# Kernel optimization log

Hardware: AMD Instinct MI355X
Metric: run time of the kernel (lower is better)

## Reference

```python
import jax, jax.numpy as jnp
import numpy as np

# dims: H heads, D=word_size (d_model), E=embed_dim per head, N=seq_len=n, K=linformer k
H, D, E, N, K = 16, 1024, 64, 4096, 256


def setup_inputs() -> dict:
    key = jax.random.key(0)
    ks = jax.random.split(key, 9)
    s = 0.02  # init scale for weights
    return {
        "x":  jax.random.normal(ks[0], (N, D), jnp.float32),
        # per-head QKV linears: torch Linear weight is (out=E, in=D), bias (E,)
        "Wq": jax.random.normal(ks[1], (H, E, D), jnp.float32) * s,
        "bq": jnp.zeros((H, E), jnp.float32),
        "Wk": jax.random.normal(ks[2], (H, E, D), jnp.float32) * s,
        "bk": jnp.zeros((H, E), jnp.float32),
        "Wv": jax.random.normal(ks[3], (H, E, D), jnp.float32) * s,
        "bv": jnp.zeros((H, E), jnp.float32),
        # per-head E/F sequence projections: Linear(n=N, k=K) -> weight (K, N), bias (K,)
        "Ew": jax.random.normal(ks[4], (H, K, N), jnp.float32) * s,
        "Eb": jnp.zeros((H, K), jnp.float32),
        "Fw": jax.random.normal(ks[5], (H, K, N), jnp.float32) * s,
        "Fb": jnp.zeros((H, K), jnp.float32),
        # output projection: Linear(H*E, E, bias=False) -> weight (E, H*E)
        "Wo": jax.random.normal(ks[6], (E, H * E), jnp.float32) * s,
    }


def reference(x, Wq, bq, Wk, bk, Wv, bv, Ew, Eb, Fw, Fb, Wo):
    # per-head Q/K/V projections, batched over heads: (H, N, E)
    q = jnp.einsum('nd,hed->hne', x, Wq) + bq[:, None, :]
    k = jnp.einsum('nd,hed->hne', x, Wk) + bk[:, None, :]
    v = jnp.einsum('nd,hed->hne', x, Wv) + bv[:, None, :]
    # low-rank sequence-length projection of K and V: (H, K, E)
    kp = jnp.einsum('hjn,hne->hje', Ew, k) + Eb[:, :, None]
    vp = jnp.einsum('hjn,hne->hje', Fw, v) + Fb[:, :, None]
    # scaled dot-product attention against projected keys: (H, N, K)
    score = jnp.einsum('hne,hje->hnj', q, kp) / jnp.sqrt(jnp.float32(E))
    attn = jax.nn.softmax(score, axis=-1)
    z = jnp.einsum('hnj,hje->hne', attn, vp)  # (H, N, E)
    # concat heads along feature dim (matches torch.cat(dim=1)): (N, H*E)
    zs = jnp.transpose(z, (1, 0, 2)).reshape(N, H * E)
    # final projection Linear(H*E, E, bias=False)
    return zs @ Wo.T  # (N, E)
```

## Files before the change

kernel.cpp:

```cpp
#include <hip/hip_runtime.h>
#include <hip/hip_bf16.h>

typedef __attribute__((ext_vector_type(4))) float f32x4;
typedef __attribute__((ext_vector_type(8))) short s16x8;
typedef __attribute__((ext_vector_type(4))) short s16x4;
typedef unsigned short u16;


__device__ __forceinline__ f32x4 mfma16(s16x8 a, s16x8 b, f32x4 c) {
    return __builtin_amdgcn_mfma_f32_16x16x32_bf16(a, b, c, 0, 0, 0);
}

__device__ __forceinline__ u16 bf(float f) {
    union { float f; unsigned u; } x; x.f = f;
    return (u16)((x.u + 0x7fffu + ((x.u >> 16) & 1u)) >> 16);
}
__device__ __forceinline__ unsigned pkbf(float a, float b) {
    union { float f; unsigned u; } x, y; x.f = a; y.f = b;
    unsigned ra = x.u + 0x7fffu + ((x.u >> 16) & 1u);
    unsigned rb = y.u + 0x7fffu + ((y.u >> 16) & 1u);
    return (ra >> 16) | (rb & 0xffff0000u);
}
__device__ __forceinline__ s16x8 cvt8(f32x4 lo, f32x4 hi) {
    union { s16x8 v; unsigned u[4]; } r;
    r.u[0] = pkbf(lo.x, lo.y);
    r.u[1] = pkbf(lo.z, lo.w);
    r.u[2] = pkbf(hi.x, hi.y);
    r.u[3] = pkbf(hi.z, hi.w);
    return r.v;
}

__device__ __forceinline__ void gl_lds16(const u16* g, u16* l) {
    __builtin_amdgcn_global_load_lds(
        (const __attribute__((address_space(1))) unsigned*)g,
        (__attribute__((address_space(3))) unsigned*)l, 16, 0, 0);
}


__global__ __launch_bounds__(256) void cvt_kernel(const float* __restrict__ src,
                                                  u16* __restrict__ dst, int n4) {
    int i = blockIdx.x * 256 + threadIdx.x;
    if (i < n4) {
        f32x4 v = ((const f32x4*)src)[i];
        union { s16x4 v; unsigned u[2]; } r;
        r.u[0] = pkbf(v.x, v.y);
        r.u[1] = pkbf(v.z, v.w);
        ((s16x4*)dst)[i] = r.v;
    }
}


__global__ __launch_bounds__(256, 2) void qkv_kernel(
        const u16* __restrict__ xb, const u16* __restrict__ wb,
        const float* __restrict__ bq, const float* __restrict__ bk,
        const float* __restrict__ bv,
        u16* __restrict__ qo, u16* __restrict__ kTo, u16* __restrict__ vTo) {
    __shared__ u16 As[128 * 32];
    __shared__ u16 Bs[128 * 32];
    int bx   = blockIdx.x % 24;
    int by   = blockIdx.x / 24;
    int tid  = threadIdx.x;
    int lane = tid & 63, w = tid >> 6;
    int l15  = lane & 15, quad = lane >> 4;
    int wr   = w >> 1, wc = w & 1;

    const u16* Ag = xb + (size_t)(by * 128 + (tid >> 2)) * 1024 + (tid & 3) * 8;
    const u16* Bg = wb + (size_t)(bx * 128 + (tid >> 2)) * 1024 + (tid & 3) * 8;
    u16* Al = As + tid * 8;
    u16* Bl = Bs + tid * 8;

    const u16* abase = As + (wr * 64 + l15) * 32 + quad * 8;
    const u16* bbase = Bs + (wc * 64 + l15) * 32 + quad * 8;

    f32x4 acc[4][4] = {};
    for (int k0 = 0; k0 < 1024; k0 += 32) {
        gl_lds16(Ag + k0, Al);
        gl_lds16(Ag + 64 * 1024 + k0, Al + 64 * 32);
        gl_lds16(Bg + k0, Bl);
        gl_lds16(Bg + 64 * 1024 + k0, Bl + 64 * 32);
        __syncthreads();
        s16x8 a[4], b[4];
#pragma unroll
        for (int mi = 0; mi < 4; mi++) a[mi] = *(const s16x8*)(abase + mi * 16 * 32);
#pragma unroll
        for (int nj = 0; nj < 4; nj++) b[nj] = *(const s16x8*)(bbase + nj * 16 * 32);
#pragma unroll
        for (int mi = 0; mi < 4; mi++)
#pragma unroll
            for (int nj = 0; nj < 4; nj++) acc[mi][nj] = mfma16(a[mi], b[nj], acc[mi][nj]);
        __syncthreads();
    }

    int fblk = (bx * 128 + wc * 64) >> 6;
    int mat  = fblk >> 4, h = fblk & 15;
    const float* bias = (mat == 0) ? bq : (mat == 1 ? bk : bv);
#pragma unroll
    for (int nj = 0; nj < 4; nj++) {
        int e = nj * 16 + l15;
        float bb = bias[h * 64 + e];
#pragma unroll
        for (int mi = 0; mi < 4; mi++) {
            int n0 = by * 128 + wr * 64 + mi * 16 + quad * 4;
            f32x4 c = acc[mi][nj];
            if (mat == 0) {
                u16* p = qo + ((size_t)h * 4096 + n0) * 64 + e;
#pragma unroll
                for (int r = 0; r < 4; r++) p[(size_t)r * 64] = bf(c[r] + bb);
            } else {
                u16* p = (mat == 1 ? kTo : vTo) + ((size_t)h * 64 + e) * 4096 + n0;
                union { s16x4 v; u16 s[4]; } pk;
#pragma unroll
                for (int r = 0; r < 4; r++) pk.s[r] = bf(c[r] + bb);
                *(s16x4*)p = pk.v;
            }
        }
    }
}


__global__ __launch_bounds__(256) void kpvp_kernel(
        const float* __restrict__ Ew, const float* __restrict__ Fw,
        const u16* __restrict__ kT, const u16* __restrict__ vT,
        float* __restrict__ accb) {
    int b    = blockIdx.x;
    int ks   = b & 7, jt = (b >> 3) & 3, h = (b >> 5) & 15, p = b >> 9;
    int lane = threadIdx.x & 63, w = threadIdx.x >> 6;
    int l15  = lane & 15, quad = lane >> 4;

    const float* A = (p ? Fw : Ew) +
        ((size_t)h * 256 + jt * 64 + w * 16 + l15) * 4096 + ks * 512 + quad * 8;
    const u16* B = (p ? vT : kT) +
        (size_t)h * 64 * 4096 + (size_t)l15 * 4096 + ks * 512 + quad * 8;

    f32x4 acc[4] = {};
    for (int k = 0; k < 512; k += 32) {
        f32x4 a0 = *(const f32x4*)(A + k);
        f32x4 a1 = *(const f32x4*)(A + k + 4);
        s16x8 av = cvt8(a0, a1);
#pragma unroll
        for (int j = 0; j < 4; j++) {
            s16x8 bv = *(const s16x8*)(B + (size_t)j * 16 * 4096 + k);
            acc[j] = mfma16(av, bv, acc[j]);
        }
    }
    float* out = accb + ((size_t)(p * 16 + h) * 256 + jt * 64 + w * 16 + quad * 4) * 64;
#pragma unroll
    for (int j = 0; j < 4; j++) {
        int e = j * 16 + l15;
#pragma unroll
        for (int r = 0; r < 4; r++) atomicAdd(out + (size_t)r * 64 + e, acc[j][r]);
    }
}


__global__ __launch_bounds__(256) void packkv_kernel(
        const float* __restrict__ accb, const float* __restrict__ Eb,
        const float* __restrict__ Fb, u16* __restrict__ kp, u16* __restrict__ vpT) {
    int idx = blockIdx.x * 256 + threadIdx.x;
    int p = idx >> 18, h = (idx >> 14) & 15, j = (idx >> 6) & 255, e = idx & 63;
    float v = accb[idx];
    if (p == 0) {
        v += Eb[h * 256 + j];
        kp[((size_t)(h * 256 + j)) * 64 + e] = bf(v * 0.125f);
    } else {
        v += Fb[h * 256 + j];
        vpT[((size_t)(h * 64 + e)) * 256 + j] = bf(v);
    }
}


__global__ __launch_bounds__(256) void attn_kernel(
        const u16* __restrict__ q, const u16* __restrict__ kp,
        const u16* __restrict__ vpT, u16* __restrict__ zs) {
    __shared__ u16 ps[4][16][256];
    int bm   = blockIdx.x & 63, h = blockIdx.x >> 6;
    int lane = threadIdx.x & 63, w = threadIdx.x >> 6;
    int l15  = lane & 15, quad = lane >> 4;
    int nbase = bm * 64 + w * 16;

    f32x4 s[16] = {};
    const u16* qp  = q  + ((size_t)h * 4096 + nbase + l15) * 64 + quad * 8;
    const u16* kpp = kp + ((size_t)h * 256 + l15) * 64 + quad * 8;
#pragma unroll
    for (int e0 = 0; e0 < 64; e0 += 32) {
        s16x8 a = *(const s16x8*)(qp + e0);
#pragma unroll
        for (int jt = 0; jt < 16; jt++) {
            s16x8 b = *(const s16x8*)(kpp + jt * 16 * 64 + e0);
            s[jt] = mfma16(a, b, s[jt]);
        }
    }

    float lsum[4];
#pragma unroll
    for (int r = 0; r < 4; r++) {
        float m = s[0][r];
#pragma unroll
        for (int jt = 1; jt < 16; jt++) m = fmaxf(m, s[jt][r]);
        m = fmaxf(m, __shfl_xor(m, 1));
        m = fmaxf(m, __shfl_xor(m, 2));
        m = fmaxf(m, __shfl_xor(m, 4));
        m = fmaxf(m, __shfl_xor(m, 8));
        float l = 0.f;
#pragma unroll
        for (int jt = 0; jt < 16; jt++) {
            float pv = __expf(s[jt][r] - m);
            s[jt][r] = pv;
            l += pv;
        }
        l += __shfl_xor(l, 1);
        l += __shfl_xor(l, 2);
        l += __shfl_xor(l, 4);
        l += __shfl_xor(l, 8);
        lsum[r] = l;
    }

#pragma unroll
    for (int jt = 0; jt < 16; jt++)
#pragma unroll
        for (int r = 0; r < 4; r++)
            ps[w][quad * 4 + r][jt * 16 + l15] = bf(s[jt][r]);
    __syncthreads();

    f32x4 z[4] = {};
    const u16* vp = vpT + ((size_t)h * 64 + l15) * 256 + quad * 8;
#pragma unroll
    for (int kj = 0; kj < 8; kj++) {
        s16x8 a = *(const s16x8*)&ps[w][l15][kj * 32 + quad * 8];
#pragma unroll
        for (int et = 0; et < 4; et++) {
            s16x8 b = *(const s16x8*)(vp + et * 16 * 256 + kj * 32);
            z[et] = mfma16(a, b, z[et]);
        }
    }
#pragma unroll
    for (int et = 0; et < 4; et++) {
        int e = et * 16 + l15;
        u16* o = zs + ((size_t)(nbase + quad * 4)) * 1024 + h * 64 + e;
#pragma unroll
        for (int r = 0; r < 4; r++) o[(size_t)r * 1024] = bf(z[et][r] / lsum[r]);
    }
}


__global__ __launch_bounds__(256) void out_kernel(
        const u16* __restrict__ zs, const u16* __restrict__ wob,
        float* __restrict__ out) {
    int ks   = blockIdx.x & 3;
    int bm   = blockIdx.x >> 2;
    int lane = threadIdx.x & 63, w = threadIdx.x >> 6;
    int l15  = lane & 15, quad = lane >> 4;
    int row0 = bm * 128 + w * 32;

    const u16* A = zs  + (size_t)(row0 + l15) * 1024 + ks * 256 + quad * 8;
    const u16* B = wob + (size_t)l15 * 1024 + ks * 256 + quad * 8;

    f32x4 acc[2][4] = {};
    for (int k = 0; k < 256; k += 32) {
        s16x8 a0 = *(const s16x8*)(A + k);
        s16x8 a1 = *(const s16x8*)(A + 16 * 1024 + k);
#pragma unroll
        for (int nt = 0; nt < 4; nt++) {
            s16x8 bv = *(const s16x8*)(B + (size_t)nt * 16 * 1024 + k);
            acc[0][nt] = mfma16(a0, bv, acc[0][nt]);
            acc[1][nt] = mfma16(a1, bv, acc[1][nt]);
        }
    }
#pragma unroll
    for (int mt = 0; mt < 2; mt++)
#pragma unroll
        for (int nt = 0; nt < 4; nt++) {
            int e = nt * 16 + l15;
            int n0 = row0 + mt * 16 + quad * 4;
            float* o = out + (size_t)n0 * 64 + e;
#pragma unroll
            for (int r = 0; r < 4; r++) atomicAdd(o + (size_t)r * 64, acc[mt][nt][r]);
        }
}


extern "C" void kernel_launch(void* const* d_in, const int* in_sizes, int n_in,
                              void* d_out, int out_size, void* d_ws, size_t ws_size,
                              hipStream_t stream) {
    const float* x  = (const float*)d_in[0];
    const float* Wq = (const float*)d_in[1];
    const float* bq = (const float*)d_in[2];
    const float* Wk = (const float*)d_in[3];
    const float* bk = (const float*)d_in[4];
    const float* Wv = (const float*)d_in[5];
    const float* bv = (const float*)d_in[6];
    const float* Ew = (const float*)d_in[7];
    const float* Eb = (const float*)d_in[8];
    const float* Fw = (const float*)d_in[9];
    const float* Fb = (const float*)d_in[10];
    const float* Wo = (const float*)d_in[11];

    char* ws = (char*)d_ws;
    u16*   qb   = (u16*)(ws + 0);
    u16*   kT   = (u16*)(ws + 8388608);
    u16*   vT   = (u16*)(ws + 16777216);
    u16*   zsb  = (u16*)(ws + 25165824);
    float* accb = (float*)(ws + 33554432);
    u16*   kp   = (u16*)(ws + 35651584);
    u16*   vpT  = (u16*)(ws + 36175872);
    u16*   xb   = (u16*)(ws + 36700160);
    u16*   wb   = (u16*)(ws + 45088768);
    u16*   wob  = (u16*)(ws + 51380224);

    hipMemsetAsync(accb, 0, (size_t)2 * 16 * 256 * 64 * sizeof(float), stream);
    hipMemsetAsync(d_out, 0, (size_t)4096 * 64 * sizeof(float), stream);

    cvt_kernel<<<4096, 256, 0, stream>>>(x,  xb, 1048576);
    cvt_kernel<<<1024, 256, 0, stream>>>(Wq, wb,           262144);
    cvt_kernel<<<1024, 256, 0, stream>>>(Wk, wb + 1048576, 262144);
    cvt_kernel<<<1024, 256, 0, stream>>>(Wv, wb + 2097152, 262144);
    cvt_kernel<<<64,   256, 0, stream>>>(Wo, wob, 16384);

    qkv_kernel<<<768, 256, 0, stream>>>(xb, wb, bq, bk, bv, qb, kT, vT);
    kpvp_kernel<<<1024, 256, 0, stream>>>(Ew, Fw, kT, vT, accb);
    packkv_kernel<<<2048, 256, 0, stream>>>(accb, Eb, Fb, kp, vpT);
    attn_kernel<<<1024, 256, 0, stream>>>(qb, kp, vpT, zsb);
    out_kernel<<<128, 256, 0, stream>>>(zsb, wob, (float*)d_out);
}
```

Before: 301.3 us.

## Stage kpvp tiles in LDS with 128-row block tiles and finer K-split

Rewrites the low-rank K/V projection kernel to stage fp32 Ew/Fw tiles (converted to bf16) and the K/V transposed tiles in shared memory. Each wave now computes a 32x64 output instead of 16x64, so B fragments are reused across two row tiles. The K dimension is split 16 ways instead of 8, and the kernel declares an occupancy hint of 4 blocks. This targets redundant global reads of B. In exchange it adds two barriers per step with no double buffering and doubles the number of atomic partial-sum writes.

New measurement: 319.8 us. +6.1%, slower.

```diff
diff --git a/kernel.cpp b/kernel.cpp
--- a/kernel.cpp
+++ b/kernel.cpp
@@ -118,38 +118,65 @@
 }
 
 
-__global__ __launch_bounds__(256) void kpvp_kernel(
+__global__ __launch_bounds__(256, 4) void kpvp_kernel(
         const float* __restrict__ Ew, const float* __restrict__ Fw,
         const u16* __restrict__ kT, const u16* __restrict__ vT,
         float* __restrict__ accb) {
+    __shared__ u16 As[128 * 32];
+    __shared__ u16 Bs[64 * 32];
     int b    = blockIdx.x;
-    int ks   = b & 7, jt = (b >> 3) & 3, h = (b >> 5) & 15, p = b >> 9;
-    int lane = threadIdx.x & 63, w = threadIdx.x >> 6;
+    int ks   = b & 15, jt = (b >> 4) & 1, h = (b >> 5) & 15, p = b >> 9;
+    int tid  = threadIdx.x;
+    int lane = tid & 63, w = tid >> 6;
     int l15  = lane & 15, quad = lane >> 4;
 
-    const float* A = (p ? Fw : Ew) +
-        ((size_t)h * 256 + jt * 64 + w * 16 + l15) * 4096 + ks * 512 + quad * 8;
-    const u16* B = (p ? vT : kT) +
-        (size_t)h * 64 * 4096 + (size_t)l15 * 4096 + ks * 512 + quad * 8;
-
-    f32x4 acc[4] = {};
-    for (int k = 0; k < 512; k += 32) {
-        f32x4 a0 = *(const f32x4*)(A + k);
-        f32x4 a1 = *(const f32x4*)(A + k + 4);
-        s16x8 av = cvt8(a0, a1);
-#pragma unroll
-        for (int j = 0; j < 4; j++) {
-            s16x8 bv = *(const s16x8*)(B + (size_t)j * 16 * 4096 + k);
-            acc[j] = mfma16(av, bv, acc[j]);
-        }
-    }
-    float* out = accb + ((size_t)(p * 16 + h) * 256 + jt * 64 + w * 16 + quad * 4) * 64;
-#pragma unroll
-    for (int j = 0; j < 4; j++) {
-        int e = j * 16 + l15;
-#pragma unroll
-        for (int r = 0; r < 4; r++) atomicAdd(out + (size_t)r * 64 + e, acc[j][r]);
-    }
+    const float* Ab = (p ? Fw : Ew) + ((size_t)h * 256 + jt * 128) * 4096 + ks * 256;
+    const u16*  Bb = (p ? vT : kT) + (size_t)h * 64 * 4096 + ks * 256;
+
+    int arow = tid >> 3, acol = (tid & 7) * 4;
+    const float* Ag = Ab + (size_t)arow * 4096 + acol;
+    u16* Aw = As + arow * 32 + acol;
+    const u16* Bg = Bb + (size_t)(tid >> 2) * 4096 + (tid & 3) * 8;
+    u16* Bl = Bs + tid * 8;
+
+    const u16* abase = As + (w * 32 + l15) * 32 + quad * 8;
+    const u16* bbase = Bs + l15 * 32 + quad * 8;
+
+    f32x4 acc[2][4] = {};
+    for (int s = 0; s < 8; s++) {
+        int kk = s * 32;
+        gl_lds16(Bg + kk, Bl);
+#pragma unroll
+        for (int ps = 0; ps < 4; ps++) {
+            f32x4 v = *(const f32x4*)(Ag + (size_t)ps * 32 * 4096 + kk);
+            union { s16x4 q; unsigned u[2]; } r;
+            r.u[0] = pkbf(v.x, v.y);
+            r.u[1] = pkbf(v.z, v.w);
+            *(s16x4*)(Aw + ps * 32 * 32) = r.q;
+        }
+        __syncthreads();
+        s16x8 a[2], bb[4];
+#pragma unroll
+        for (int mi = 0; mi < 2; mi++) a[mi] = *(const s16x8*)(abase + mi * 16 * 32);
+#pragma unroll
+        for (int nj = 0; nj < 4; nj++) bb[nj] = *(const s16x8*)(bbase + nj * 16 * 32);
+#pragma unroll
+        for (int mi = 0; mi < 2; mi++)
+#pragma unroll
+            for (int nj = 0; nj < 4; nj++) acc[mi][nj] = mfma16(a[mi], bb[nj], acc[mi][nj]);
+        __syncthreads();
+    }
+
+    float* out = accb + ((size_t)(p * 16 + h) * 256 + jt * 128 + w * 32 + quad * 4) * 64;
+#pragma unroll
+    for (int mi = 0; mi < 2; mi++)
+#pragma unroll
+        for (int nj = 0; nj < 4; nj++) {
+            int e = nj * 16 + l15;
+#pragma unroll
+            for (int r = 0; r < 4; r++)
+                atomicAdd(out + (size_t)(mi * 16 + r) * 64 + e, acc[mi][nj][r]);
+        }
 }
 
 
```

## Restructure kpvp split-K GEMM with double-buffered LDS tiles and deterministic partial sums

Applied to the files above, without the earlier changes.

Rewrites the Ew/Fw-by-K/V sequence-projection GEMM to stage tiles in LDS with double buffering, using direct global-to-LDS loads for the bf16 operand and fp32-to-bf16 conversion into LDS for the weight operand. The split-K factor drops from 8 to 4 and the per-block j tile narrows. Each split now writes its own partial buffer instead of doing fp32 atomics, so the accumulator memset goes away and packkv sums the four partials. The aim is to cut redundant global reads of B across waves and atomic contention, at the cost of a larger workspace and extra partial-buffer traffic.

After: 313.2 us. +3.9%, slower.

```diff
diff --git a/kernel.cpp b/kernel.cpp
--- a/kernel.cpp
+++ b/kernel.cpp
@@ -118,47 +118,82 @@
 }
 
 
-__global__ __launch_bounds__(256) void kpvp_kernel(
+__global__ __launch_bounds__(256, 4) void kpvp_kernel(
         const float* __restrict__ Ew, const float* __restrict__ Fw,
         const u16* __restrict__ kT, const u16* __restrict__ vT,
-        float* __restrict__ accb) {
+        float* __restrict__ accs) {
+    __shared__ u16 As[2][32 * 72];
+    __shared__ u16 Bs[2][8192];
     int b    = blockIdx.x;
-    int ks   = b & 7, jt = (b >> 3) & 3, h = (b >> 5) & 15, p = b >> 9;
-    int lane = threadIdx.x & 63, w = threadIdx.x >> 6;
+    int ks   = b & 3, jt = (b >> 2) & 7, h = (b >> 5) & 15, p = b >> 9;
+    int tid  = threadIdx.x;
+    int lane = tid & 63, w = tid >> 6;
     int l15  = lane & 15, quad = lane >> 4;
-
-    const float* A = (p ? Fw : Ew) +
-        ((size_t)h * 256 + jt * 64 + w * 16 + l15) * 4096 + ks * 512 + quad * 8;
-    const u16* B = (p ? vT : kT) +
-        (size_t)h * 64 * 4096 + (size_t)l15 * 4096 + ks * 512 + quad * 8;
-
-    f32x4 acc[4] = {};
-    for (int k = 0; k < 512; k += 32) {
-        f32x4 a0 = *(const f32x4*)(A + k);
-        f32x4 a1 = *(const f32x4*)(A + k + 4);
-        s16x8 av = cvt8(a0, a1);
-#pragma unroll
-        for (int j = 0; j < 4; j++) {
-            s16x8 bv = *(const s16x8*)(B + (size_t)j * 16 * 4096 + k);
-            acc[j] = mfma16(av, bv, acc[j]);
-        }
-    }
-    float* out = accb + ((size_t)(p * 16 + h) * 256 + jt * 64 + w * 16 + quad * 4) * 64;
-#pragma unroll
-    for (int j = 0; j < 4; j++) {
-        int e = j * 16 + l15;
-#pragma unroll
-        for (int r = 0; r < 4; r++) atomicAdd(out + (size_t)r * 64 + e, acc[j][r]);
-    }
+    int wm   = w & 1, wn = w >> 1;
+
+    const float* Ag = (p ? Fw : Ew) +
+        ((size_t)(h * 256 + jt * 32) + (tid >> 3)) * 4096 + ks * 1024 + (tid & 7) * 8;
+    const u16* Bg = (p ? vT : kT) +
+        ((size_t)h * 64 + (tid >> 2)) * 4096 + ks * 1024 + (tid & 3) * 8;
+
+    u16* Aw[2] = { &As[0][(tid >> 3) * 72 + (tid & 7) * 8],
+                   &As[1][(tid >> 3) * 72 + (tid & 7) * 8] };
+    u16* Bw[2] = { &Bs[0][tid * 8], &Bs[1][tid * 8] };
+
+    gl_lds16(Bg, Bw[0]);
+    gl_lds16(Bg + 32, Bw[0] + 4096);
+    {
+        f32x4 a0 = *(const f32x4*)(Ag);
+        f32x4 a1 = *(const f32x4*)(Ag + 4);
+        *(s16x8*)Aw[0] = cvt8(a0, a1);
+    }
+
+    const u16* abase = &As[0][(wm * 16 + l15) * 72 + quad * 8];
+    const u16* bbase = &Bs[0][(wn * 32 + l15) * 32 + quad * 8];
+
+    f32x4 acc[2] = {};
+    for (int s = 0; s < 16; s++) {
+        __syncthreads();
+        int cur = s & 1, nxt = cur ^ 1;
+        f32x4 a0, a1;
+        if (s < 15) {
+            gl_lds16(Bg + (s + 1) * 64, Bw[nxt]);
+            gl_lds16(Bg + (s + 1) * 64 + 32, Bw[nxt] + 4096);
+            a0 = *(const f32x4*)(Ag + (s + 1) * 64);
+            a1 = *(const f32x4*)(Ag + (s + 1) * 64 + 4);
+        }
+        const u16* ab = abase + cur * (32 * 72);
+        const u16* bb = bbase + cur * 8192;
+#pragma unroll
+        for (int kstep = 0; kstep < 2; kstep++) {
+            s16x8 af = *(const s16x8*)(ab + kstep * 32);
+#pragma unroll
+            for (int nt = 0; nt < 2; nt++) {
+                s16x8 bfr = *(const s16x8*)(bb + kstep * 4096 + nt * 16 * 32);
+                acc[nt] = mfma16(af, bfr, acc[nt]);
+            }
+        }
+        if (s < 15) {
+            *(s16x8*)Aw[nxt] = cvt8(a0, a1);
+        }
+    }
+
+    size_t base = (size_t)ks * 524288 +
+        ((size_t)(p * 16 + h) * 256 + jt * 32 + wm * 16 + quad * 4) * 64 + wn * 32 + l15;
+#pragma unroll
+    for (int nt = 0; nt < 2; nt++)
+#pragma unroll
+        for (int r = 0; r < 4; r++)
+            accs[base + (size_t)r * 64 + nt * 16] = acc[nt][r];
 }
 
 
 __global__ __launch_bounds__(256) void packkv_kernel(
-        const float* __restrict__ accb, const float* __restrict__ Eb,
+        const float* __restrict__ accs, const float* __restrict__ Eb,
         const float* __restrict__ Fb, u16* __restrict__ kp, u16* __restrict__ vpT) {
     int idx = blockIdx.x * 256 + threadIdx.x;
+    float v = accs[idx] + accs[idx + 524288] + accs[idx + 1048576] + accs[idx + 1572864];
     int p = idx >> 18, h = (idx >> 14) & 15, j = (idx >> 6) & 255, e = idx & 63;
-    float v = accb[idx];
     if (p == 0) {
         v += Eb[h * 256 + j];
         kp[((size_t)(h * 256 + j)) * 64 + e] = bf(v * 0.125f);
@@ -300,14 +335,13 @@
     u16*   kT   = (u16*)(ws + 8388608);
     u16*   vT   = (u16*)(ws + 16777216);
     u16*   zsb  = (u16*)(ws + 25165824);
-    float* accb = (float*)(ws + 33554432);
-    u16*   kp   = (u16*)(ws + 35651584);
-    u16*   vpT  = (u16*)(ws + 36175872);
-    u16*   xb   = (u16*)(ws + 36700160);
-    u16*   wb   = (u16*)(ws + 45088768);
-    u16*   wob  = (u16*)(ws + 51380224);
-
-    hipMemsetAsync(accb, 0, (size_t)2 * 16 * 256 * 64 * sizeof(float), stream);
+    float* accs = (float*)(ws + 33554432);
+    u16*   kp   = (u16*)(ws + 41943040);
+    u16*   vpT  = (u16*)(ws + 42467328);
+    u16*   xb   = (u16*)(ws + 42991616);
+    u16*   wb   = (u16*)(ws + 51380224);
+    u16*   wob  = (u16*)(ws + 57671680);
+
     hipMemsetAsync(d_out, 0, (size_t)4096 * 64 * sizeof(float), stream);
 
     cvt_kernel<<<4096, 256, 0, stream>>>(x,  xb, 1048576);
@@ -317,8 +351,8 @@
     cvt_kernel<<<64,   256, 0, stream>>>(Wo, wob, 16384);
 
     qkv_kernel<<<768, 256, 0, stream>>>(xb, wb, bq, bk, bv, qb, kT, vT);
-    kpvp_kernel<<<1024, 256, 0, stream>>>(Ew, Fw, kT, vT, accb);
-    packkv_kernel<<<2048, 256, 0, stream>>>(accb, Eb, Fb, kp, vpT);
+    kpvp_kernel<<<1024, 256, 0, stream>>>(Ew, Fw, kT, vT, accs);
+    packkv_kernel<<<2048, 256, 0, stream>>>(accs, Eb, Fb, kp, vpT);
     attn_kernel<<<1024, 256, 0, stream>>>(qb, kp, vpT, zsb);
     out_kernel<<<128, 256, 0, stream>>>(zsb, wob, (float*)d_out);
 }
```
